# Kernel tuning notes

Hardware: AMD Instinct MI355X
Metric: run time of the kernel (lower is better)

Reference implementation:

```python
import jax, jax.numpy as jnp
import numpy as np

B, T, H, V = 64, 128, 50, 8192  # batch, window, lstm hidden (=embedding_size=50 in source), vocab
REC_DROP, DENSE_DROP = 0.3, 0.5


def setup_inputs() -> dict:
    key = jax.random.key(0)
    ks = jax.random.split(key, 16)
    n = lambda k, *s: 0.1 * jax.random.normal(k, s, dtype=jnp.float32)
    inp = {}
    inp["batched_input"] = jax.random.randint(ks[0], (B, T), 0, V)
    inp["E"] = n(ks[1], V, H)                  # embedding table
    inp["Wx"] = n(ks[2], H, 4 * H)             # LSTM input kernel (i,f,c,o)
    inp["U"] = n(ks[3], 4, H, H)               # LSTM recurrent kernel per gate
    inp["b"] = jnp.zeros((4 * H,), jnp.float32)
    inp["W1"] = n(ks[4], H, V)                 # denseTypeOne, first application
    inp["b1"] = jnp.zeros((V,), jnp.float32)   # shared bias (layer reused)
    inp["W1b"] = n(ks[5], V, V)                # denseTypeOne, second application (V->V)
    inp["W2"] = n(ks[6], V, V)                 # denseTypeTwo (sigmoid)
    inp["b2"] = jnp.zeros((V,), jnp.float32)
    # Frozen dropout masks (inverted-dropout scaling baked in).
    inp["rec_mask"] = jax.random.bernoulli(ks[7], 1.0 - REC_DROP, (4, B, H)).astype(jnp.float32) / (1.0 - REC_DROP)
    inp["dmask1"] = jax.random.bernoulli(ks[8], 1.0 - DENSE_DROP, (B, T // 2, V)).astype(jnp.float32) / (1.0 - DENSE_DROP)
    inp["dmask2"] = jax.random.bernoulli(ks[9], 1.0 - DENSE_DROP, (B, T // 2, V)).astype(jnp.float32) / (1.0 - DENSE_DROP)
    return inp


def _lstm(emb, Wx, U, b, rec_mask):
    # emb: [B,T,H]; precompute input contribution once, scan over time.
    zx = jnp.einsum('bth,hk->tbk', emb, Wx) + b  # [T,B,4H]

    def step(carry, z_t):
        h, c = carry
        # per-gate recurrent dropout on h, as Keras does off the cuDNN path
        rec = jnp.einsum('gbh,ghk->bgk', h[None, :, :] * rec_mask, U)  # [B,4,H]
        z = z_t.reshape(B, 4, H) + rec
        i = jax.nn.sigmoid(z[:, 0])
        f = jax.nn.sigmoid(z[:, 1])
        g = jnp.tanh(z[:, 2])
        o = jax.nn.sigmoid(z[:, 3])
        c_new = f * c + i * g
        h_new = o * jnp.tanh(c_new)
        return (h_new, c_new), h_new

    init = (jnp.zeros((B, H), emb.dtype), jnp.zeros((B, H), emb.dtype))
    _, hs = jax.lax.scan(step, init, zx)  # [T,B,H]
    return jnp.transpose(hs, (1, 0, 2))   # [B,T,H]


def reference(batched_input, E, Wx, U, b, W1, b1, W1b, W2, b2, rec_mask, dmask1, dmask2):
    emb = E[batched_input]                       # [B,T,H]
    seq = _lstm(emb, Wx, U, b, rec_mask)         # [B,T,H]
    pooled = seq.reshape(B, T // 2, 2, H).max(axis=2)  # MaxPool1D(pool=2)
    d1 = jax.nn.relu(pooled @ W1 + b1)           # [B,T/2,V]
    x = d1 * dmask1                              # dropout 0.5 (training=True)
    d2 = jax.nn.relu(x @ W1b + b1)               # denseTypeOne reused (shared bias)
    x = d2 * dmask2
    prbs = jax.nn.sigmoid(x @ W2 + b2)           # [B,T/2,V]
    return prbs
```

## Files before the change

kernel.cpp:

```cpp
#include <hip/hip_runtime.h>


#define Bc 64
#define Tc 128
#define Hc 50
#define Vc 8192
#define Mrows 4096

typedef unsigned short u16;
typedef short bf16x8 __attribute__((ext_vector_type(8)));
typedef float f32x4 __attribute__((ext_vector_type(4)));

__device__ __forceinline__ u16 f2bf(float x) {
  union { float f; unsigned int u; } v; v.f = x;
  unsigned int r = v.u + 0x7fffu + ((v.u >> 16) & 1u);
  return (u16)(r >> 16);
}

__device__ __forceinline__ void async_copy16(void* lds, const void* g) {
  __builtin_amdgcn_global_load_lds(
      (const __attribute__((address_space(1))) void*)g,
      (__attribute__((address_space(3))) void*)lds, 16, 0, 0);
}

__device__ __forceinline__ float sigmoidf(float x) {
  return 1.0f / (1.0f + __expf(-x));
}

__global__ __launch_bounds__(256) void zx_kernel(
    const int* __restrict__ tok, const float* __restrict__ E,
    const float* __restrict__ Wx, const float* __restrict__ bvec,
    float* __restrict__ zx) {
  const int tb = blockIdx.x;
  const int t = tb >> 6, b = tb & 63;
  __shared__ float e_s[Hc];
  const int id = tok[b * Tc + t];
  if (threadIdx.x < Hc) e_s[threadIdx.x] = E[id * Hc + threadIdx.x];
  __syncthreads();
  if (threadIdx.x < 4 * Hc) {
    float acc = bvec[threadIdx.x];
    #pragma unroll
    for (int h = 0; h < Hc; ++h) acc += e_s[h] * Wx[h * 200 + threadIdx.x];
    zx[(size_t)tb * 200 + threadIdx.x] = acc;
  }
}

__global__ __launch_bounds__(256) void lstm_kernel(
    const float* __restrict__ zx, const float* __restrict__ U,
    const float* __restrict__ rec_mask, u16* __restrict__ pooled) {
  const int b = blockIdx.x;
  const int tid = threadIdx.x;
  __shared__ float Us[4 * Hc * Hc];
  __shared__ float recm[4 * Hc];
  __shared__ float h_s[Hc], c_s[Hc], hprev[Hc];
  __shared__ float hm[4 * Hc], z_s[4 * Hc];

  for (int i = tid; i < 4 * Hc * Hc; i += 256) Us[i] = U[i];
  if (tid < 200) recm[tid] = rec_mask[(tid / Hc) * Bc * Hc + b * Hc + (tid % Hc)];
  if (tid < Hc) { h_s[tid] = 0.f; c_s[tid] = 0.f; }
  __syncthreads();

  for (int t = 0; t < Tc; ++t) {
    if (tid < 200) hm[tid] = h_s[tid % Hc] * recm[tid];
    __syncthreads();
    if (tid < 200) {
      const int g = tid / Hc, k = tid % Hc;
      float acc = zx[((size_t)t * Bc + b) * 200 + tid];
      const float* Ug = Us + g * Hc * Hc;
      const float* hmg = hm + g * Hc;
      #pragma unroll
      for (int h = 0; h < Hc; ++h) acc += hmg[h] * Ug[h * Hc + k];
      z_s[tid] = acc;
    }
    __syncthreads();
    if (tid < Hc) {
      const int k = tid;
      const float i_ = sigmoidf(z_s[k]);
      const float f_ = sigmoidf(z_s[Hc + k]);
      const float g_ = tanhf(z_s[2 * Hc + k]);
      const float o_ = sigmoidf(z_s[3 * Hc + k]);
      const float c = f_ * c_s[k] + i_ * g_;
      const float h = o_ * tanhf(c);
      c_s[k] = c; h_s[k] = h;
      if ((t & 1) != 0) {
        pooled[((size_t)b * 64 + (t >> 1)) * 64 + k] = f2bf(fmaxf(hprev[k], h));
      } else {
        hprev[k] = h;
      }
    }
    if ((t & 1) != 0 && tid >= Hc && tid < 64)
      pooled[((size_t)b * 64 + (t >> 1)) * 64 + tid] = 0;
    __syncthreads();
  }
}

__global__ __launch_bounds__(256) void w1t_kernel(
    const float* __restrict__ W1, u16* __restrict__ W1T) {
  const int idx = blockIdx.x * 256 + threadIdx.x;
  const int n = idx >> 6, k = idx & 63;
  const float v = (k < Hc) ? W1[(size_t)k * Vc + n] : 0.f;
  W1T[idx] = f2bf(v);
}

__global__ __launch_bounds__(256) void wt_kernel(
    const float* __restrict__ W, u16* __restrict__ WT) {
  __shared__ float sm[128][65];
  const int t = threadIdx.x;
  const size_t k0 = (size_t)blockIdx.x * 128;
  const size_t n0 = (size_t)blockIdx.y * 64;
  {
    const int n = t & 63, kr = t >> 6;
    #pragma unroll
    for (int i = 0; i < 32; ++i) {
      const int k = i * 4 + kr;
      sm[k][n] = W[(k0 + k) * Vc + n0 + n];
    }
  }
  __syncthreads();
  {
    const int kk = (t & 63) * 2, nr = t >> 6;
    #pragma unroll
    for (int i = 0; i < 16; ++i) {
      const int nn = i * 4 + nr;
      ushort2 v;
      v.x = f2bf(sm[kk][nn]);
      v.y = f2bf(sm[kk + 1][nn]);
      *(ushort2*)&WT[(n0 + nn) * Vc + k0 + kk] = v;
    }
  }
}

template <bool SIGMOID>
__global__ __launch_bounds__(256, 2) void gemm_bt(
    const u16* __restrict__ A, const u16* __restrict__ Bt,
    const float* __restrict__ bias, const float* __restrict__ mask,
    void* __restrict__ Cout, const int M, const int N, const int K) {
  __shared__ u16 As[128 * 64];
  __shared__ u16 Bs[128 * 64];
  const int tid = threadIdx.x;
  const int wave = tid >> 6;
  const int lane = tid & 63;
  const int wr = (wave >> 1) << 6;
  const int wc = (wave & 1) << 6;
  const long tileM = (long)blockIdx.y * 128;
  const long tileN = (long)blockIdx.x * 128;

  const int lrow = lane >> 3;
  const int cg8 = (((lane & 7) ^ lrow) << 3);
  const u16* Ab = A + tileM * K;
  const u16* Bb = Bt + tileN * K;

  f32x4 acc[4][4] = {};

  for (int k0 = 0; k0 < K; k0 += 64) {
    #pragma unroll
    for (int q4 = 0; q4 < 4; ++q4) {
      const int r = (wave << 5) + (q4 << 3) + lrow;
      const int ldsoff = (wave * 4 + q4) << 10;
      async_copy16((char*)As + ldsoff, Ab + (long)r * K + k0 + cg8);
      async_copy16((char*)Bs + ldsoff, Bb + (long)r * K + k0 + cg8);
    }
    __syncthreads();
    #pragma unroll
    for (int kk = 0; kk < 64; kk += 32) {
      const int ch = (kk >> 3) + (lane >> 4);
      bf16x8 af[4], bf[4];
      #pragma unroll
      for (int i = 0; i < 4; ++i) {
        const int ra = wr + (i << 4) + (lane & 15);
        af[i] = *(const bf16x8*)(As + ra * 64 + ((ch ^ (ra & 7)) << 3));
      }
      #pragma unroll
      for (int j = 0; j < 4; ++j) {
        const int rb = wc + (j << 4) + (lane & 15);
        bf[j] = *(const bf16x8*)(Bs + rb * 64 + ((ch ^ (rb & 7)) << 3));
      }
      #pragma unroll
      for (int i = 0; i < 4; ++i)
        #pragma unroll
        for (int j = 0; j < 4; ++j)
          acc[i][j] = __builtin_amdgcn_mfma_f32_16x16x32_bf16(af[i], bf[j], acc[i][j], 0, 0, 0);
    }
    __syncthreads();
  }

  const int qrow = (lane >> 4) << 2;
  const int qcol = lane & 15;
  #pragma unroll
  for (int j = 0; j < 4; ++j) {
    const long col = tileN + wc + (j << 4) + qcol;
    const float bv = bias[col];
    #pragma unroll
    for (int i = 0; i < 4; ++i) {
      const long row0 = tileM + wr + (i << 4) + qrow;
      #pragma unroll
      for (int r = 0; r < 4; ++r) {
        const long off = (row0 + r) * N + col;
        const float z = acc[i][j][r] + bv;
        if constexpr (SIGMOID) {
          ((float*)Cout)[off] = sigmoidf(z);
        } else {
          ((u16*)Cout)[off] = f2bf(fmaxf(z, 0.f) * mask[off]);
        }
      }
    }
  }
}

extern "C" void kernel_launch(void* const* d_in, const int* in_sizes, int n_in,
                              void* d_out, int out_size, void* d_ws, size_t ws_size,
                              hipStream_t stream) {
  const int*   tok  = (const int*)  d_in[0];
  const float* E    = (const float*)d_in[1];
  const float* Wx   = (const float*)d_in[2];
  const float* U    = (const float*)d_in[3];
  const float* bvec = (const float*)d_in[4];
  const float* W1   = (const float*)d_in[5];
  const float* b1   = (const float*)d_in[6];
  const float* W1b  = (const float*)d_in[7];
  const float* W2   = (const float*)d_in[8];
  const float* b2   = (const float*)d_in[9];
  const float* recm = (const float*)d_in[10];
  const float* dm1  = (const float*)d_in[11];
  const float* dm2  = (const float*)d_in[12];
  float* out = (float*)d_out;

  char* w = (char*)d_ws;
  u16* Wt     = (u16*)w;  w += (size_t)Vc * Vc * 2;
  u16* A1     = (u16*)w;  w += (size_t)Mrows * Vc * 2;
  u16* A2     = (u16*)w;  w += (size_t)Mrows * Vc * 2;
  u16* W1T    = (u16*)w;  w += (size_t)Vc * 64 * 2;
  u16* pooled = (u16*)w;  w += (size_t)Mrows * 64 * 2;
  float* zx   = (float*)w;

  zx_kernel  <<<Bc * Tc, 256, 0, stream>>>(tok, E, Wx, bvec, zx);
  lstm_kernel<<<Bc, 256, 0, stream>>>(zx, U, recm, pooled);
  w1t_kernel <<<(Vc * 64) / 256, 256, 0, stream>>>(W1, W1T);
  gemm_bt<false><<<dim3(Vc / 128, Mrows / 128), 256, 0, stream>>>(
      pooled, W1T, b1, dm1, A1, Mrows, Vc, 64);
  wt_kernel<<<dim3(Vc / 128, Vc / 64), 256, 0, stream>>>(W1b, Wt);
  gemm_bt<false><<<dim3(Vc / 128, Mrows / 128), 256, 0, stream>>>(
      A1, Wt, b1, dm2, A2, Mrows, Vc, Vc);
  wt_kernel<<<dim3(Vc / 128, Vc / 64), 256, 0, stream>>>(W2, Wt);
  gemm_bt<true><<<dim3(Vc / 128, Mrows / 128), 256, 0, stream>>>(
      A2, Wt, b2, nullptr, out, Mrows, Vc, Vc);
}
```

Before: 2.046 ms.

## Use 256x256 double-buffered pipelined GEMM for the two large VxV layers

Adds a 512-thread GEMM kernel with 256x256 output tiles, double-buffered LDS, and async global-to-LDS staging interleaved with MFMA phases using explicit waitcnt, barriers and setprio. It also swizzles block IDs into groups of eight for better L2 locality. The aim is to raise operand reuse per LDS load and hide memory latency in the two 4096x8192x8192 GEMMs that dominate runtime. The cost is heavier register pressure from 32 accumulators per thread and hand-tuned synchronization that could stall or race if the wait counts are wrong.

```diff
diff --git a/kernel.cpp b/kernel.cpp
--- a/kernel.cpp
+++ b/kernel.cpp
@@ -201,6 +201,142 @@
           ((float*)Cout)[off] = sigmoidf(z);
         } else {
           ((u16*)Cout)[off] = f2bf(fmaxf(z, 0.f) * mask[off]);
+        }
+      }
+    }
+  }
+}
+
+template <bool SIGMOID>
+__global__ __launch_bounds__(512, 2) void gemm256(
+    const u16* __restrict__ A, const u16* __restrict__ Bt,
+    const float* __restrict__ bias, const float* __restrict__ mask,
+    void* __restrict__ Cout, const int M, const int N, const int K) {
+  __shared__ u16 As[2][16384];
+  __shared__ u16 Bs[2][16384];
+  const int tid = threadIdx.x;
+  const int wave = tid >> 6;
+  const int lane = tid & 63;
+  const int l15 = lane & 15;
+  const int chb = lane >> 4;
+  const int wm64 = ((wave >> 2) & 1) << 6;
+  const int wn32 = (wave & 3) << 5;
+
+  const int nwg = gridDim.x;
+  const int cpx = nwg >> 3;
+  const int bid = blockIdx.x;
+  const int swz = (bid & 7) * cpx + (bid >> 3);
+  const int ntN = N >> 8;
+  const long tileM = (long)(swz / ntN) << 8;
+  const long tileN = (long)(swz % ntN) << 8;
+
+  const u16* Ab = A + tileM * K;
+  const u16* Bb = Bt + tileN * K;
+
+  const int srow = tid >> 3;
+  const int schunk = ((tid & 7) ^ (srow & 7)) << 3;
+  const long srowK = (long)srow * K + schunk;
+  const long K64 = (long)K << 6;
+  const int stgoff = wave << 10;
+  const int nt = K >> 6;
+
+  f32x4 acc[8][4] = {};
+
+#define STG(DSTBASE, SRCB, KT, HH) do {                                   \
+    const int _kt = (KT) < nt ? (KT) : nt - 1;                            \
+    const u16* _s = (SRCB) + ((long)(HH) * 128) * K + srowK + ((long)_kt << 6); \
+    char* _d = (char*)(DSTBASE) + (HH) * 16384 + stgoff;                  \
+    async_copy16(_d, _s);                                                 \
+    async_copy16(_d + 8192, _s + K64);                                    \
+  } while (0)
+
+  STG(As[0], Ab, 0, 0);
+  STG(Bs[0], Bb, 0, 0);
+  STG(As[0], Ab, 0, 1);
+  STG(Bs[0], Bb, 0, 1);
+  STG(As[1], Ab, 1, 0);
+  STG(Bs[1], Bb, 1, 0);
+  asm volatile("s_waitcnt vmcnt(8)" ::: "memory");
+  __builtin_amdgcn_s_barrier();
+
+#define PHASE(CUR, MH, NH, STAGE_STMT, WAIT_STMT) do {                    \
+    bf16x8 af[2][4], bv[2][2];                                            \
+    const u16* _A = As[CUR];                                              \
+    const u16* _B = Bs[CUR];                                              \
+    _Pragma("unroll")                                                     \
+    for (int kc = 0; kc < 2; ++kc) {                                      \
+      const int ch = (kc << 2) + chb;                                     \
+      _Pragma("unroll")                                                   \
+      for (int i = 0; i < 4; ++i) {                                       \
+        const int ra = (MH) * 128 + wm64 + (i << 4) + l15;                \
+        af[kc][i] = *(const bf16x8*)(_A + ra * 64 + ((ch ^ (ra & 7)) << 3)); \
+      }                                                                   \
+      _Pragma("unroll")                                                   \
+      for (int j = 0; j < 2; ++j) {                                       \
+        const int rb = (NH) * 128 + wn32 + (j << 4) + l15;                \
+        bv[kc][j] = *(const bf16x8*)(_B + rb * 64 + ((ch ^ (rb & 7)) << 3)); \
+      }                                                                   \
+    }                                                                     \
+    STAGE_STMT;                                                           \
+    __builtin_amdgcn_s_barrier();                                         \
+    asm volatile("s_waitcnt lgkmcnt(0)" ::: "memory");                    \
+    __builtin_amdgcn_sched_barrier(0);                                    \
+    __builtin_amdgcn_s_setprio(1);                                        \
+    _Pragma("unroll")                                                     \
+    for (int kc = 0; kc < 2; ++kc)                                        \
+      _Pragma("unroll")                                                   \
+      for (int i = 0; i < 4; ++i)                                         \
+        _Pragma("unroll")                                                 \
+        for (int j = 0; j < 2; ++j)                                       \
+          acc[(MH) * 4 + i][(NH) * 2 + j] =                               \
+              __builtin_amdgcn_mfma_f32_16x16x32_bf16(                    \
+                  af[kc][i], bv[kc][j], acc[(MH) * 4 + i][(NH) * 2 + j],  \
+                  0, 0, 0);                                               \
+    __builtin_amdgcn_s_setprio(0);                                        \
+    WAIT_STMT;                                                            \
+    __builtin_amdgcn_s_barrier();                                         \
+  } while (0)
+
+  for (int T = 0; T < nt; T += 2) {
+    PHASE(0, 0, 0, STG(As[1], Ab, T + 1, 1),
+          asm volatile("s_waitcnt vmcnt(6)" ::: "memory"));
+    PHASE(0, 0, 1, STG(Bs[1], Bb, T + 1, 1), (void)0);
+    PHASE(0, 1, 0, STG(As[0], Ab, T + 2, 0), (void)0);
+    PHASE(0, 1, 1, STG(Bs[0], Bb, T + 2, 0),
+          asm volatile("s_waitcnt vmcnt(8)" ::: "memory"));
+    PHASE(1, 0, 0, STG(As[0], Ab, T + 2, 1),
+          asm volatile("s_waitcnt vmcnt(6)" ::: "memory"));
+    PHASE(1, 0, 1, STG(Bs[0], Bb, T + 2, 1), (void)0);
+    PHASE(1, 1, 0, STG(As[1], Ab, T + 3, 0), (void)0);
+    PHASE(1, 1, 1, STG(Bs[1], Bb, T + 3, 0),
+          asm volatile("s_waitcnt vmcnt(8)" ::: "memory"));
+  }
+
+#undef PHASE
+#undef STG
+
+  const int qrow = (lane >> 4) << 2;
+  #pragma unroll
+  for (int nh = 0; nh < 2; ++nh) {
+    #pragma unroll
+    for (int j = 0; j < 2; ++j) {
+      const long col = tileN + nh * 128 + wn32 + (j << 4) + l15;
+      const float bvv = bias[col];
+      #pragma unroll
+      for (int mh = 0; mh < 2; ++mh) {
+        #pragma unroll
+        for (int i = 0; i < 4; ++i) {
+          const long row0 = tileM + mh * 128 + wm64 + (i << 4) + qrow;
+          #pragma unroll
+          for (int r = 0; r < 4; ++r) {
+            const long off = (row0 + r) * N + col;
+            const float z = acc[mh * 4 + i][nh * 2 + j][r] + bvv;
+            if constexpr (SIGMOID) {
+              ((float*)Cout)[off] = sigmoidf(z);
+            } else {
+              ((u16*)Cout)[off] = f2bf(fmaxf(z, 0.f) * mask[off]);
+            }
+          }
         }
       }
     }
@@ -239,9 +375,9 @@
   gemm_bt<false><<<dim3(Vc / 128, Mrows / 128), 256, 0, stream>>>(
       pooled, W1T, b1, dm1, A1, Mrows, Vc, 64);
   wt_kernel<<<dim3(Vc / 128, Vc / 64), 256, 0, stream>>>(W1b, Wt);
-  gemm_bt<false><<<dim3(Vc / 128, Mrows / 128), 256, 0, stream>>>(
+  gemm256<false><<<dim3((Mrows / 256) * (Vc / 256)), 512, 0, stream>>>(
       A1, Wt, b1, dm2, A2, Mrows, Vc, Vc);
   wt_kernel<<<dim3(Vc / 128, Vc / 64), 256, 0, stream>>>(W2, Wt);
-  gemm_bt<true><<<dim3(Vc / 128, Mrows / 128), 256, 0, stream>>>(
+  gemm256<true><<<dim3((Mrows / 256) * (Vc / 256)), 512, 0, stream>>>(
       A2, Wt, b2, nullptr, out, Mrows, Vc, Vc);
 }
```

New measurement: 2.283 ms. 11.6% more time.
